# Performance work log

Hardware: AMD Instinct MI355X
Metric: run time of the kernel (lower is better)

The kernel has to match this reference:

```python
import jax, jax.numpy as jnp
import numpy as np

NH = 12  # num_heads

def setup_inputs() -> dict:
    key = jax.random.key(0)
    ks = jax.random.split(key, 8)
    B, N, C = 8, 1024, 768
    d = C // NH  # head_dim == qk_head_dim (qk_head_dim=None)
    s = 0.02
    return {
        "x": jax.random.normal(ks[0], (B, N, C), jnp.float32),
        "Wq": jax.random.normal(ks[1], (C, NH * d), jnp.float32) * s,
        "Wk": jax.random.normal(ks[2], (C, NH * d), jnp.float32) * s,
        "Wv": jax.random.normal(ks[3], (C, C), jnp.float32) * s,
        "Wproj": jax.random.normal(ks[4], (C, C), jnp.float32) * s,
        "proj_b": jax.random.normal(ks[5], (C,), jnp.float32) * s,
        "attn_bias": jax.random.normal(ks[6], (N, N), jnp.float32) * s,
        "head_bias": jax.random.normal(ks[7], (NH, N, N), jnp.float32) * s,
    }

def reference(x, Wq, Wk, Wv, Wproj, proj_b, attn_bias, head_bias):
    B, N, C = x.shape
    d = C // NH
    scale = d ** -0.5
    # projections: [B,N,C] -> [B,nh,N,d]
    q = jnp.einsum('bnc,ce->bne', x, Wq).reshape(B, N, NH, d).transpose(0, 2, 1, 3)
    k = jnp.einsum('bnc,ce->bne', x, Wk).reshape(B, N, NH, d).transpose(0, 2, 1, 3)
    v = jnp.einsum('bnc,ce->bne', x, Wv).reshape(B, N, NH, d).transpose(0, 2, 1, 3)
    # scaled scores + global bias + per-head bias
    scores = jnp.einsum('bhnd,bhmd->bhnm', q * scale, k)
    scores = scores + attn_bias[None, None] + head_bias[None]
    attn = jax.nn.softmax(scores, axis=-1)  # [B,nh,N,N]
    out = jnp.einsum('bhnm,bhmd->bhnd', attn, v)
    out = out.transpose(0, 2, 1, 3).reshape(B, N, C)
    out = jnp.einsum('bnc,ce->bne', out, Wproj) + proj_b
    return out, attn
```

## Files before the change

### kernel.cpp

```cpp
#include <hip/hip_runtime.h>
#include <cstddef>

#define B_   8
#define N_   1024
#define C_   768
#define NH_  12
#define HD_  64
#define M_   (B_ * N_)

typedef __attribute__((ext_vector_type(8))) short  short8;
typedef __attribute__((ext_vector_type(4))) float  f32x4;

__device__ __forceinline__ unsigned short f2b(float f) {
    union { float f; unsigned u; } v; v.f = f;
    unsigned u = v.u;
    return (unsigned short)((u + 0x7FFFu + ((u >> 16) & 1u)) >> 16);
}
__device__ __forceinline__ float b2f(unsigned short s) {
    union { unsigned u; float f; } v; v.u = ((unsigned)s) << 16;
    return v.f;
}

__global__ __launch_bounds__(256) void cast_x_kernel(const float* __restrict__ x,
                                                     unsigned short* __restrict__ xb) {
    const int n4 = M_ * C_ / 4;
    for (int i = blockIdx.x * blockDim.x + threadIdx.x; i < n4; i += gridDim.x * blockDim.x) {
        float4 v = ((const float4*)x)[i];
        ushort4 o;
        o.x = f2b(v.x); o.y = f2b(v.y); o.z = f2b(v.z); o.w = f2b(v.w);
        ((ushort4*)xb)[i] = o;
    }
}

__global__ __launch_bounds__(256) void bias_combine_kernel(
    const float* __restrict__ ab, const float* __restrict__ hbias,
    unsigned short* __restrict__ bc) {
    const int total4 = NH_ * N_ * N_ / 4;
    const int qm4 = N_ * N_ / 4;
    for (int i = blockIdx.x * blockDim.x + threadIdx.x; i < total4; i += gridDim.x * blockDim.x) {
        int rem = i % qm4;
        float4 a = ((const float4*)ab)[rem];
        float4 h = ((const float4*)hbias)[i];
        ushort4 o;
        o.x = f2b(a.x + h.x); o.y = f2b(a.y + h.y);
        o.z = f2b(a.z + h.z); o.w = f2b(a.w + h.w);
        ((ushort4*)bc)[i] = o;
    }
}

__global__ __launch_bounds__(256) void transpose_cast_kernel(
    const float* __restrict__ w0, const float* __restrict__ w1,
    const float* __restrict__ w2, const float* __restrict__ w3,
    unsigned short* __restrict__ t0, unsigned short* __restrict__ t1,
    unsigned short* __restrict__ t2, unsigned short* __restrict__ t3) {
    const int z = blockIdx.z;
    const float* src = (z == 0) ? w0 : (z == 1) ? w1 : (z == 2) ? w2 : w3;
    unsigned short* dst = (z == 0) ? t0 : (z == 1) ? t1 : (z == 2) ? t2 : t3;
    __shared__ float tile[32][33];
    const int r0 = blockIdx.y * 32, c0 = blockIdx.x * 32;
    const int tx = threadIdx.x & 31, ty = threadIdx.x >> 5;
    #pragma unroll
    for (int p = 0; p < 4; ++p)
        tile[ty + 8 * p][tx] = src[(size_t)(r0 + ty + 8 * p) * C_ + c0 + tx];
    __syncthreads();
    #pragma unroll
    for (int p = 0; p < 4; ++p)
        dst[(size_t)(c0 + ty + 8 * p) * C_ + r0 + tx] = f2b(tile[tx][ty + 8 * p]);
}

__global__ __launch_bounds__(256) void qkv_gemm(
    const unsigned short* __restrict__ A,
    const unsigned short* __restrict__ W0, const unsigned short* __restrict__ W1,
    const unsigned short* __restrict__ W2,
    unsigned short* __restrict__ o0, unsigned short* __restrict__ o1,
    unsigned short* __restrict__ o2) {
    __shared__ unsigned short As[128][40];
    __shared__ unsigned short Bs[64][40];
    const int z = blockIdx.z;
    const unsigned short* Bt = (z == 0) ? W0 : (z == 1) ? W1 : W2;
    const int tid = threadIdx.x;
    const int wid = tid >> 6, lane = tid & 63;
    const int ln = lane & 15, g = lane >> 4;
    const int wm = wid >> 1, wn = wid & 1;
    const int bm = blockIdx.y * 128, bn = blockIdx.x * 64;

    f32x4 acc[4][2];
    #pragma unroll
    for (int i = 0; i < 4; ++i)
        #pragma unroll
        for (int j = 0; j < 2; ++j) acc[i][j] = (f32x4)0.f;

    for (int k0 = 0; k0 < C_; k0 += 32) {
        #pragma unroll
        for (int p = 0; p < 2; ++p) {
            int idx = tid + p * 256;
            int row = idx >> 2, ch = idx & 3;
            *(int4*)&As[row][ch * 8] =
                *(const int4*)&A[(size_t)(bm + row) * C_ + k0 + ch * 8];
        }
        {
            int n = tid >> 2, ch = tid & 3;
            *(int4*)&Bs[n][ch * 8] =
                *(const int4*)&Bt[(size_t)(bn + n) * C_ + k0 + ch * 8];
        }
        __syncthreads();
        short8 a[4], b[2];
        #pragma unroll
        for (int mt = 0; mt < 4; ++mt)
            a[mt] = *(const short8*)&As[wm * 64 + mt * 16 + ln][g * 8];
        #pragma unroll
        for (int nt = 0; nt < 2; ++nt)
            b[nt] = *(const short8*)&Bs[wn * 32 + nt * 16 + ln][g * 8];
        #pragma unroll
        for (int mt = 0; mt < 4; ++mt)
            #pragma unroll
            for (int nt = 0; nt < 2; ++nt)
                acc[mt][nt] = __builtin_amdgcn_mfma_f32_16x16x32_bf16(
                    a[mt], b[nt], acc[mt][nt], 0, 0, 0);
        __syncthreads();
    }

    unsigned short* outp = (z == 0) ? o0 : (z == 1) ? o1 : o2;
    #pragma unroll
    for (int mt = 0; mt < 4; ++mt) {
        #pragma unroll
        for (int nt = 0; nt < 2; ++nt) {
            f32x4 c = acc[mt][nt];
            int rowb = bm + wm * 64 + mt * 16 + g * 4;
            int col  = bn + wn * 32 + nt * 16 + ln;
            int hh = col >> 6, dd = col & 63;
            if (z < 2) {
                #pragma unroll
                for (int i = 0; i < 4; ++i) {
                    int row = rowb + i;
                    int bb = row >> 10, n = row & 1023;
                    outp[((size_t)(bb * NH_ + hh) * N_ + n) * HD_ + dd] = f2b(c[i]);
                }
            } else {
                int bb = rowb >> 10, n0 = rowb & 1023;
                ushort4 pk;
                pk.x = f2b(c[0]); pk.y = f2b(c[1]); pk.z = f2b(c[2]); pk.w = f2b(c[3]);
                *(ushort4*)&outp[((size_t)(bb * NH_ + hh) * HD_ + dd) * N_ + n0] = pk;
            }
        }
    }
}

__global__ __launch_bounds__(256) void proj_gemm(
    const unsigned short* __restrict__ A, const unsigned short* __restrict__ Bt,
    const float* __restrict__ bias, float* __restrict__ outp) {
    __shared__ unsigned short As[128][40];
    __shared__ unsigned short Bs[64][40];
    const int tid = threadIdx.x;
    const int wid = tid >> 6, lane = tid & 63;
    const int ln = lane & 15, g = lane >> 4;
    const int wm = wid >> 1, wn = wid & 1;
    const int bm = blockIdx.y * 128, bn = blockIdx.x * 64;

    f32x4 acc[4][2];
    #pragma unroll
    for (int i = 0; i < 4; ++i)
        #pragma unroll
        for (int j = 0; j < 2; ++j) acc[i][j] = (f32x4)0.f;

    for (int k0 = 0; k0 < C_; k0 += 32) {
        #pragma unroll
        for (int p = 0; p < 2; ++p) {
            int idx = tid + p * 256;
            int row = idx >> 2, ch = idx & 3;
            *(int4*)&As[row][ch * 8] =
                *(const int4*)&A[(size_t)(bm + row) * C_ + k0 + ch * 8];
        }
        {
            int n = tid >> 2, ch = tid & 3;
            *(int4*)&Bs[n][ch * 8] =
                *(const int4*)&Bt[(size_t)(bn + n) * C_ + k0 + ch * 8];
        }
        __syncthreads();
        short8 a[4], b[2];
        #pragma unroll
        for (int mt = 0; mt < 4; ++mt)
            a[mt] = *(const short8*)&As[wm * 64 + mt * 16 + ln][g * 8];
        #pragma unroll
        for (int nt = 0; nt < 2; ++nt)
            b[nt] = *(const short8*)&Bs[wn * 32 + nt * 16 + ln][g * 8];
        #pragma unroll
        for (int mt = 0; mt < 4; ++mt)
            #pragma unroll
            for (int nt = 0; nt < 2; ++nt)
                acc[mt][nt] = __builtin_amdgcn_mfma_f32_16x16x32_bf16(
                    a[mt], b[nt], acc[mt][nt], 0, 0, 0);
        __syncthreads();
    }

    #pragma unroll
    for (int mt = 0; mt < 4; ++mt) {
        #pragma unroll
        for (int nt = 0; nt < 2; ++nt) {
            f32x4 c = acc[mt][nt];
            int rowb = bm + wm * 64 + mt * 16 + g * 4;
            int col  = bn + wn * 32 + nt * 16 + ln;
            float bb = bias[col];
            #pragma unroll
            for (int i = 0; i < 4; ++i)
                outp[(size_t)(rowb + i) * C_ + col] = c[i] + bb;
        }
    }
}

__global__ __launch_bounds__(512) void attn_fused(
    const unsigned short* __restrict__ qh, const unsigned short* __restrict__ kh,
    const unsigned short* __restrict__ vt,
    const unsigned short* __restrict__ bias_c,
    float* __restrict__ attn_out, unsigned short* __restrict__ hb) {
    __shared__ unsigned short sc[32 * 1024];
    __shared__ float sinv[32];
    const int b = blockIdx.x, qb0 = blockIdx.y * 32, h = blockIdx.z;
    const int bh = b * NH_ + h;
    const int tid = threadIdx.x;
    const int wid = tid >> 6, lane = tid & 63;
    const int ln = lane & 15, g = lane >> 4;

    #define SCP(row, m) ((unsigned short*)((char*)sc + (row) * 2048 + \
                         (((m) * 2) ^ (((row) & 7) << 4))))

    {
        short8 qf[2][2];
        #pragma unroll
        for (int Mt = 0; Mt < 2; ++Mt)
            #pragma unroll
            for (int kc = 0; kc < 2; ++kc)
                qf[Mt][kc] = *(const short8*)&qh[
                    ((size_t)bh * N_ + qb0 + Mt * 16 + ln) * HD_ + kc * 32 + g * 8];
        const int mb = wid * 128;
        const unsigned short* kbase = kh + (size_t)bh * N_ * HD_;
        short8 k0 = *(const short8*)&kbase[(size_t)(mb + ln) * HD_ + g * 8];
        short8 k1 = *(const short8*)&kbase[(size_t)(mb + ln) * HD_ + 32 + g * 8];
        for (int mt = 0; mt < 8; ++mt) {
            const int m0 = mb + mt * 16;
            const int m1 = (mt < 7) ? m0 + 16 : m0;
            short8 n0 = *(const short8*)&kbase[(size_t)(m1 + ln) * HD_ + g * 8];
            short8 n1 = *(const short8*)&kbase[(size_t)(m1 + ln) * HD_ + 32 + g * 8];
            #pragma unroll
            for (int Mt = 0; Mt < 2; ++Mt) {
                f32x4 s = (f32x4)0.f;
                s = __builtin_amdgcn_mfma_f32_16x16x32_bf16(k0, qf[Mt][0], s, 0, 0, 0);
                s = __builtin_amdgcn_mfma_f32_16x16x32_bf16(k1, qf[Mt][1], s, 0, 0, 0);
                const int q = qb0 + Mt * 16 + ln;
                const int mrow = m0 + g * 4;
                ushort4 bc = *(const ushort4*)&bias_c[((size_t)h * N_ + q) * N_ + mrow];
                ushort4 pk;
                pk.x = f2b(fmaf(s[0], 0.125f, b2f(bc.x)));
                pk.y = f2b(fmaf(s[1], 0.125f, b2f(bc.y)));
                pk.z = f2b(fmaf(s[2], 0.125f, b2f(bc.z)));
                pk.w = f2b(fmaf(s[3], 0.125f, b2f(bc.w)));
                *(ushort4*)SCP(Mt * 16 + ln, mrow) = pk;
            }
            k0 = n0; k1 = n1;
        }
    }
    __syncthreads();

    {
        const int r = tid >> 4, t16 = tid & 15;
        ushort4 er[16];
        float mx = -1e30f;
        #pragma unroll
        for (int j = 0; j < 16; ++j) {
            er[j] = *(const ushort4*)SCP(r, t16 * 4 + j * 64);
            mx = fmaxf(fmaxf(fmaxf(mx, b2f(er[j].x)), fmaxf(b2f(er[j].y), b2f(er[j].z))),
                       b2f(er[j].w));
        }
        #pragma unroll
        for (int off = 8; off; off >>= 1) mx = fmaxf(mx, __shfl_xor(mx, off, 16));
        float sum = 0.f;
        #pragma unroll
        for (int j = 0; j < 16; ++j) {
            float4 e;
            e.x = __expf(b2f(er[j].x) - mx);
            e.y = __expf(b2f(er[j].y) - mx);
            e.z = __expf(b2f(er[j].z) - mx);
            e.w = __expf(b2f(er[j].w) - mx);
            sum += e.x + e.y + e.z + e.w;
            er[j].x = f2b(e.x); er[j].y = f2b(e.y);
            er[j].z = f2b(e.z); er[j].w = f2b(e.w);
            *(ushort4*)SCP(r, t16 * 4 + j * 64) = er[j];
        }
        #pragma unroll
        for (int off = 8; off; off >>= 1) sum += __shfl_xor(sum, off, 16);
        const float inv = 1.f / sum;
        if (t16 == 0) sinv[r] = inv;
        float* arow = attn_out + ((size_t)bh * N_ + qb0 + r) * N_;
        #pragma unroll
        for (int j = 0; j < 16; ++j) {
            f32x4 o;
            o[0] = b2f(er[j].x) * inv;
            o[1] = b2f(er[j].y) * inv;
            o[2] = b2f(er[j].z) * inv;
            o[3] = b2f(er[j].w) * inv;
            __builtin_nontemporal_store(o, (f32x4*)&arow[t16 * 4 + j * 64]);
        }
    }
    __syncthreads();

    {
        const int Mt = wid >> 2, nt = wid & 3;
        const unsigned short* vrow = vt + ((size_t)bh * HD_ + nt * 16 + ln) * N_;
        f32x4 acc = (f32x4)0.f;
        short8 pa = *(const short8*)SCP(Mt * 16 + ln, g * 8);
        short8 vb = *(const short8*)&vrow[g * 8];
        for (int kt = 0; kt < 32; ++kt) {
            const int knext = (kt < 31) ? kt + 1 : kt;
            short8 npa = *(const short8*)SCP(Mt * 16 + ln, knext * 32 + g * 8);
            short8 nvb = *(const short8*)&vrow[knext * 32 + g * 8];
            acc = __builtin_amdgcn_mfma_f32_16x16x32_bf16(pa, vb, acc, 0, 0, 0);
            pa = npa; vb = nvb;
        }
        #pragma unroll
        for (int i = 0; i < 4; ++i) {
            int q = qb0 + Mt * 16 + g * 4 + i;
            float o = acc[i] * sinv[Mt * 16 + g * 4 + i];
            hb[(size_t)((b << 10) + q) * C_ + h * HD_ + nt * 16 + ln] = f2b(o);
        }
    }
    #undef SCP
}

extern "C" void kernel_launch(void* const* d_in, const int* in_sizes, int n_in,
                              void* d_out, int out_size, void* d_ws, size_t ws_size,
                              hipStream_t stream) {
    const float* x         = (const float*)d_in[0];
    const float* Wq        = (const float*)d_in[1];
    const float* Wk        = (const float*)d_in[2];
    const float* Wv        = (const float*)d_in[3];
    const float* Wproj     = (const float*)d_in[4];
    const float* proj_b    = (const float*)d_in[5];
    const float* attn_bias = (const float*)d_in[6];
    const float* head_bias = (const float*)d_in[7];

    float* out  = (float*)d_out;
    float* attn = out + (size_t)B_ * N_ * C_;

    unsigned short* ws = (unsigned short*)d_ws;
    const size_t SZ_X = (size_t)M_ * C_;
    const size_t SZ_W = (size_t)C_ * C_;
    unsigned short* xb  = ws;
    unsigned short* wqt = xb + SZ_X;
    unsigned short* wkt = wqt + SZ_W;
    unsigned short* wvt = wkt + SZ_W;
    unsigned short* wpt = wvt + SZ_W;
    unsigned short* qh  = wpt + SZ_W;
    unsigned short* khd = qh + SZ_X;
    unsigned short* vtp = khd + SZ_X;
    unsigned short* bc  = vtp + SZ_X;
    unsigned short* hb  = xb;

    cast_x_kernel<<<2048, 256, 0, stream>>>(x, xb);
    bias_combine_kernel<<<2048, 256, 0, stream>>>(attn_bias, head_bias, bc);
    transpose_cast_kernel<<<dim3(24, 24, 4), 256, 0, stream>>>(
        Wq, Wk, Wv, Wproj, wqt, wkt, wvt, wpt);

    qkv_gemm<<<dim3(C_ / 64, M_ / 128, 3), 256, 0, stream>>>(
        xb, wqt, wkt, wvt, qh, khd, vtp);

    attn_fused<<<dim3(B_, N_ / 32, NH_), 512, 0, stream>>>(
        qh, khd, vtp, bc, attn, hb);

    proj_gemm<<<dim3(C_ / 64, M_ / 128), 256, 0, stream>>>(hb, wpt, proj_b, out);
}
```

Baseline: 323.6 us.

## Remap attention blocks across XCDs and move bias add into softmax pass

The 3D grid is flattened to 1D, and block ids are remapped so the eight batches sharing a (query-block, head) bias tile land on the same XCD. The aim is better L2 reuse of the combined bias across batches. The bias add also moves out of the QK^T MFMA loop into the softmax pass, where it is read as coalesced row segments instead of scattered 4-element column reads. The bias is now loaded twice per row (max pass and exp pass), and the scores stored in shared memory are rounded to bf16 before the bias is added, which changes rounding slightly.

Result: faster. 310.3 us (-4.1%).

```diff
diff --git a/kernel.cpp b/kernel.cpp
--- a/kernel.cpp
+++ b/kernel.cpp
@@ -215,7 +215,12 @@
     float* __restrict__ attn_out, unsigned short* __restrict__ hb) {
     __shared__ unsigned short sc[32 * 1024];
     __shared__ float sinv[32];
-    const int b = blockIdx.x, qb0 = blockIdx.y * 32, h = blockIdx.z;
+    const int id = blockIdx.x;
+    const int xcd = id & 7;
+    const int b = (id >> 3) & 7;
+    const int qbh = ((id >> 6) << 3) + xcd;
+    const int qb0 = (qbh / NH_) * 32;
+    const int h = qbh % NH_;
     const int bh = b * NH_ + h;
     const int tid = threadIdx.x;
     const int wid = tid >> 6, lane = tid & 63;
@@ -246,14 +251,12 @@
                 f32x4 s = (f32x4)0.f;
                 s = __builtin_amdgcn_mfma_f32_16x16x32_bf16(k0, qf[Mt][0], s, 0, 0, 0);
                 s = __builtin_amdgcn_mfma_f32_16x16x32_bf16(k1, qf[Mt][1], s, 0, 0, 0);
-                const int q = qb0 + Mt * 16 + ln;
                 const int mrow = m0 + g * 4;
-                ushort4 bc = *(const ushort4*)&bias_c[((size_t)h * N_ + q) * N_ + mrow];
                 ushort4 pk;
-                pk.x = f2b(fmaf(s[0], 0.125f, b2f(bc.x)));
-                pk.y = f2b(fmaf(s[1], 0.125f, b2f(bc.y)));
-                pk.z = f2b(fmaf(s[2], 0.125f, b2f(bc.z)));
-                pk.w = f2b(fmaf(s[3], 0.125f, b2f(bc.w)));
+                pk.x = f2b(s[0] * 0.125f);
+                pk.y = f2b(s[1] * 0.125f);
+                pk.z = f2b(s[2] * 0.125f);
+                pk.w = f2b(s[3] * 0.125f);
                 *(ushort4*)SCP(Mt * 16 + ln, mrow) = pk;
             }
             k0 = n0; k1 = n1;
@@ -263,24 +266,30 @@
 
     {
         const int r = tid >> 4, t16 = tid & 15;
+        const unsigned short* brow = bias_c + ((size_t)h * N_ + qb0 + r) * N_;
         ushort4 er[16];
         float mx = -1e30f;
         #pragma unroll
         for (int j = 0; j < 16; ++j) {
             er[j] = *(const ushort4*)SCP(r, t16 * 4 + j * 64);
-            mx = fmaxf(fmaxf(fmaxf(mx, b2f(er[j].x)), fmaxf(b2f(er[j].y), b2f(er[j].z))),
-                       b2f(er[j].w));
+            ushort4 bb = *(const ushort4*)&brow[t16 * 4 + j * 64];
+            float s0 = b2f(er[j].x) + b2f(bb.x);
+            float s1 = b2f(er[j].y) + b2f(bb.y);
+            float s2 = b2f(er[j].z) + b2f(bb.z);
+            float s3 = b2f(er[j].w) + b2f(bb.w);
+            mx = fmaxf(fmaxf(fmaxf(mx, s0), fmaxf(s1, s2)), s3);
         }
         #pragma unroll
         for (int off = 8; off; off >>= 1) mx = fmaxf(mx, __shfl_xor(mx, off, 16));
         float sum = 0.f;
         #pragma unroll
         for (int j = 0; j < 16; ++j) {
+            ushort4 bb = *(const ushort4*)&brow[t16 * 4 + j * 64];
             float4 e;
-            e.x = __expf(b2f(er[j].x) - mx);
-            e.y = __expf(b2f(er[j].y) - mx);
-            e.z = __expf(b2f(er[j].z) - mx);
-            e.w = __expf(b2f(er[j].w) - mx);
+            e.x = __expf(b2f(er[j].x) + b2f(bb.x) - mx);
+            e.y = __expf(b2f(er[j].y) + b2f(bb.y) - mx);
+            e.z = __expf(b2f(er[j].z) + b2f(bb.z) - mx);
+            e.w = __expf(b2f(er[j].w) + b2f(bb.w) - mx);
             sum += e.x + e.y + e.z + e.w;
             er[j].x = f2b(e.x); er[j].y = f2b(e.y);
             er[j].z = f2b(e.z); er[j].w = f2b(e.w);
@@ -363,7 +372,7 @@
     qkv_gemm<<<dim3(C_ / 64, M_ / 128, 3), 256, 0, stream>>>(
         xb, wqt, wkt, wvt, qh, khd, vtp);
 
-    attn_fused<<<dim3(B_, N_ / 32, NH_), 512, 0, stream>>>(
+    attn_fused<<<dim3(B_ * (N_ / 32) * NH_), 512, 0, stream>>>(
         qh, khd, vtp, bc, attn, hb);
 
     proj_gemm<<<dim3(C_ / 64, M_ / 128), 256, 0, stream>>>(hb, wpt, proj_b, out);
```
